# Optimization experiments

Measured on AMD Instinct MI355X. Metric: run time of the kernel, lower is better.

The kernel has to match this reference:

```python
import jax, jax.numpy as jnp
import numpy as np

WS = 8        # window_size
NH = 16       # num_heads
EPS = 1e-5    # BatchNorm eps (inference mode: running_mean=0, running_var=1)

def conv2d(x, w, padding=0, groups=1):
    return jax.lax.conv_general_dilated(
        x, w, (1, 1), [(padding, padding), (padding, padding)],
        dimension_numbers=('NCHW', 'OIHW', 'NCHW'), feature_group_count=groups)

def bn(x, gamma, beta):
    # eval-mode BatchNorm with running_mean=0, running_var=1
    return x * (gamma / jnp.sqrt(1.0 + EPS))[None, :, None, None] + beta[None, :, None, None]

def avgpool(x, kh, kw, ph, pw):
    # torch AvgPool2d with count_include_pad=True: sum over zero-padded window / (kh*kw)
    s = jax.lax.reduce_window(x, 0.0, jax.lax.add, (1, 1, kh, kw), (1, 1, 1, 1),
                              [(0, 0), (0, 0), (ph, ph), (pw, pw)])
    return s / float(kh * kw)

def rel_pos_index(ws):
    coords = np.stack(np.meshgrid(np.arange(ws), np.arange(ws), indexing='ij')).reshape(2, -1)
    rel = (coords[:, :, None] - coords[:, None, :]).transpose(1, 2, 0) + (ws - 1)
    return (rel[..., 0] * (2 * ws - 1) + rel[..., 1]).reshape(-1)

def hge_kernels(W):
    # build 4 directional Sobel kernels + Gaussian-Laplacian from learned scalars
    S0, S45, S90 = W[:, :, 0, 0], W[:, :, 0, 1], W[:, :, 0, 2]
    S135, GL = W[:, :, 1, 0], W[:, :, 2, 2]
    z = jnp.zeros_like(S0)
    k3 = lambda rows: jnp.stack([jnp.stack(r, -1) for r in rows], -2)  # [O,I,3,3]
    w0 = k3([[S0, 2*S0, S0], [z, z, z], [-S0, -2*S0, -S0]])
    w45 = k3([[2*S45, S45, z], [S45, z, -S45], [z, -S45, -2*S45]])
    w90 = k3([[S90, z, -S90], [2*S90, z, -2*S90], [S90, z, -S90]])
    w135 = k3([[z, -S135, -2*S135], [S135, z, -S135], [2*S135, S135, z]])
    a1 = GL * 4.0; a2 = -a1 / 8.0; a3 = -a1 / 16.0
    wGL = jnp.zeros(S0.shape + (5, 5), S0.dtype)
    for i, j, v in [(0,2,a3),(1,1,a3),(1,2,a2),(1,3,a3),(2,0,a3),(2,1,a2),(2,2,a1),
                    (2,3,a2),(2,4,a3),(3,1,a3),(3,2,a2),(3,3,a3),(4,2,a3)]:
        wGL = wGL.at[:, :, i, j].set(v)
    return w0, w45, w90, w135, wGL

def forward(x, ca_h1, ca_w1, ca_fh, ca_fw, l1_w, l1_g, l1_b, l2_w, l2_g, l2_b,
            hge_w, hge_fc_w, hge_fc_b, qkv_w, rel_table, proj_dw, proj_g, proj_b, proj_pw):
    B, C, H, W = x.shape
    d = C // NH
    scale = d ** -0.5
    # --- CA block: coordinate attention (1x1 convs on H- and W-pooled features) ---
    cm = lambda w, t: jnp.einsum('oc,bc...->bo...', w, t)
    s_h = jax.nn.sigmoid(cm(ca_fh, cm(ca_h1, x.mean(3))))   # [B,C,H]
    s_w = jax.nn.sigmoid(cm(ca_fw, cm(ca_w1, x.mean(2))))   # [B,C,W]
    x = x * s_h[:, :, :, None] * s_w[:, :, None, :]
    # --- local branch: 1x1 ConvBN + 3x3 ConvBN + HGE edge operator ---
    local = bn(conv2d(x, l2_w), l2_g, l2_b) + bn(conv2d(x, l1_w, padding=1), l1_g, l1_b)
    w0, w45, w90, w135, wGL = hge_kernels(hge_w)
    feats = jnp.concatenate([conv2d(x, w0, 1), conv2d(x, w45, 1), conv2d(x, w90, 1),
                             conv2d(x, w135, 1), conv2d(x, wGL, 2)], axis=1)  # [B,5C,H,W]
    local = local + conv2d(feats, hge_fc_w) + hge_fc_b[None, :, None, None]
    # --- windowed attention ---
    ph, pw = (-H) % WS, (-W) % WS
    if ph or pw:
        x = jnp.pad(x, ((0, 0), (0, 0), (0, ph), (0, pw)), mode='reflect')
    Hp, Wp = x.shape[2], x.shape[3]
    hh, ww = Hp // WS, Wp // WS
    qkv = conv2d(x, qkv_w)                                   # [B,3C,Hp,Wp]
    qkv = qkv.reshape(B, 3, NH, d, hh, WS, ww, WS)
    qkv = qkv.transpose(1, 0, 4, 6, 2, 5, 7, 3).reshape(3, B * hh * ww, NH, WS * WS, d)
    q, k, v = qkv[0], qkv[1], qkv[2]
    bias = rel_table[rel_pos_index(WS)].reshape(WS * WS, WS * WS, NH).transpose(2, 0, 1)
    dots = jnp.einsum('wnid,wnjd->wnij', q, k) * scale + bias[None]
    attn = jax.nn.softmax(dots, axis=-1)
    o = jnp.einsum('wnij,wnjd->wnid', attn, v)
    o = o.reshape(B, hh, ww, NH, WS, WS, d).transpose(0, 3, 6, 1, 4, 2, 5)
    o = o.reshape(B, C, Hp, Wp)[:, :, :H, :W]
    # --- directional average pooling of attention output ---
    ox = avgpool(jnp.pad(o, ((0, 0), (0, 0), (0, 1), (0, 0)), mode='reflect'), WS, 1, WS // 2 - 1, 0)
    oy = avgpool(jnp.pad(o, ((0, 0), (0, 0), (0, 0), (0, 1)), mode='reflect'), 1, WS, 0, WS // 2 - 1)
    out = ox + oy + local
    # --- pad_out + separable ConvBN projection (depthwise k=ws -> BN -> 1x1) ---
    out = jnp.pad(out, ((0, 0), (0, 0), (0, 1), (0, 1)), mode='reflect')
    out = conv2d(out, proj_dw, padding=(WS - 1) // 2, groups=C)
    out = bn(out, proj_g, proj_b)
    out = conv2d(out, proj_pw)
    return out[:, :, :H, :W]

def setup_inputs() -> dict:
    key = jax.random.key(0)
    ks = jax.random.split(key, 20)
    C = 128
    f32 = jnp.float32
    n = lambda k, sh, s: jax.random.normal(k, sh, f32) * s
    return {
        'x': jax.random.normal(ks[0], (2, C, 256, 256), f32),
        'ca_h1': n(ks[1], (C, C), 0.05), 'ca_w1': n(ks[2], (C, C), 0.05),
        'ca_fh': n(ks[3], (C, C), 0.05), 'ca_fw': n(ks[4], (C, C), 0.05),
        'l1_w': n(ks[5], (C, C, 3, 3), 0.03),
        'l1_g': 1.0 + n(ks[6], (C,), 0.02), 'l1_b': n(ks[7], (C,), 0.02),
        'l2_w': n(ks[8], (C, C, 1, 1), 0.09),
        'l2_g': 1.0 + n(ks[9], (C,), 0.02), 'l2_b': n(ks[10], (C,), 0.02),
        'hge_w': n(ks[11], (C, C, 3, 3), 0.02),
        'hge_fc_w': n(ks[12], (C, 5 * C, 1, 1), 0.02), 'hge_fc_b': n(ks[13], (C,), 0.02),
        'qkv_w': n(ks[14], (3 * C, C, 1, 1), 0.05),
        'rel_table': n(ks[15], ((2 * WS - 1) ** 2, NH), 0.02),
        'proj_dw': n(ks[16], (C, 1, WS, WS), 0.05),
        'proj_g': 1.0 + n(ks[17], (C,), 0.02), 'proj_b': n(ks[18], (C,), 0.02),
        'proj_pw': n(ks[19], (C, C, 1, 1), 0.05),
    }

def reference(x, ca_h1, ca_w1, ca_fh, ca_fw, l1_w, l1_g, l1_b, l2_w, l2_g, l2_b,
              hge_w, hge_fc_w, hge_fc_b, qkv_w, rel_table, proj_dw, proj_g, proj_b, proj_pw):
    return forward(x, ca_h1, ca_w1, ca_fh, ca_fw, l1_w, l1_g, l1_b, l2_w, l2_g, l2_b,
                   hge_w, hge_fc_w, hge_fc_b, qkv_w, rel_table, proj_dw, proj_g, proj_b, proj_pw)
```

## Files before the change

kernel.cpp:

```cpp
#include <hip/hip_runtime.h>

#define BB 2
#define CC 128
#define HWSZ 65536
#define RSQE 0.9999950000374997f
#define ATT_SCALE 0.35355339059327373f

typedef unsigned short u16;
using short8 = __attribute__((ext_vector_type(8))) short;
using f32x4  = __attribute__((ext_vector_type(4))) float;

#if defined(__has_builtin)
# if __has_builtin(__builtin_amdgcn_fdot2_f32_bf16)
#  define HAVE_DOT2 1
# endif
#endif

__device__ __forceinline__ float b2f(u16 u){
  return __uint_as_float(((unsigned int)u) << 16);
}
__device__ __forceinline__ u16 f2b(float f){
  unsigned int v = __float_as_uint(f);
  unsigned int r = (v + 0x7FFFu + ((v >> 16) & 1u)) >> 16;
  return (u16)r;
}

__device__ const int c_DI[13] = {-2,-1,-1,-1, 0, 0,0,0,0, 1,1,1, 2};
__device__ const int c_DJ[13] = { 0,-1, 0, 1,-2,-1,0,1,2,-1,0,1, 0};

__global__ void k_detect(const u16* __restrict__ xr, int* __restrict__ flag){
  __shared__ int ws_[4];
  int tid = threadIdx.x;
  int cnt = 0;
  for (int i = 0; i < 16; ++i){
    u16 u = xr[tid*16 + i];
    int e = (u >> 7) & 0xFF;
    cnt += (e < 100 || e > 141) ? 1 : 0;
  }
  #pragma unroll
  for (int off = 32; off > 0; off >>= 1) cnt += __shfl_down(cnt, off, 64);
  if ((tid & 63) == 0) ws_[tid >> 6] = cnt;
  __syncthreads();
  if (tid == 0) *flag = (ws_[0]+ws_[1]+ws_[2]+ws_[3] > 64) ? 1 : 0;
}

__global__ void k_ingest4(const void* __restrict__ src, u16* __restrict__ dst,
                          int n4, const int* __restrict__ flag){
  int i = blockIdx.x * 256 + threadIdx.x;
  if (i >= n4) return;
  if (*flag){
    float4 f = ((const float4*)src)[i];
    ushort4 r; r.x=f2b(f.x); r.y=f2b(f.y); r.z=f2b(f.z); r.w=f2b(f.w);
    ((ushort4*)dst)[i] = r;
  } else {
    ((ushort4*)dst)[i] = ((const ushort4*)src)[i];
  }
}

struct PtrL { const void* p[19]; };

__global__ void k_ingest_w(PtrL pl, u16* __restrict__ dst, const int* __restrict__ flag){
  const int ends[19] = {16384,32768,49152,65536,212992,213120,213248,229632,229760,
                        229888,377344,459264,459392,508544,512144,520336,520464,520592,536976};
  int g = blockIdx.x * 256 + threadIdx.x;
  int idx = g * 4;
  if (idx >= 536976) return;
  int seg = 0, start = 0;
  #pragma unroll
  for (int s = 0; s < 19; ++s){ if (idx >= ends[s]){ seg = s+1; start = ends[s]; } }
  int local = idx - start;
  const void* sp = pl.p[seg];
  if (*flag){
    float4 f = ((const float4*)sp)[local >> 2];
    ushort4 r; r.x=f2b(f.x); r.y=f2b(f.y); r.z=f2b(f.z); r.w=f2b(f.w);
    *(ushort4*)(dst + idx) = r;
  } else {
    *(ushort4*)(dst + idx) = ((const ushort4*)sp)[local >> 2];
  }
}

__global__ void k_prep_A(const u16* __restrict__ fh, const u16* __restrict__ h1,
                         const u16* __restrict__ fw, const u16* __restrict__ w1,
                         const u16* __restrict__ l1b, const u16* __restrict__ l2b,
                         const u16* __restrict__ fcb,
                         float* __restrict__ A_h, float* __restrict__ A_w,
                         float* __restrict__ biasK){
  int idx = blockIdx.x * 256 + threadIdx.x;
  int o = idx >> 7, c = idx & 127;
  float ah = 0.f, aw = 0.f;
  for (int m = 0; m < 128; ++m){
    ah += b2f(fh[o*128 + m]) * b2f(h1[m*128 + c]);
    aw += b2f(fw[o*128 + m]) * b2f(w1[m*128 + c]);
  }
  A_h[idx] = ah; A_w[idx] = aw;
  if (c == 0) biasK[o] = b2f(l1b[o]) + b2f(l2b[o]) + b2f(fcb[o]);
}

__global__ void k_prep_rel(const u16* __restrict__ rel, float* __restrict__ relo){
  int idx = blockIdx.x * 256 + threadIdx.x;
  if (idx >= 3600) return;
  int head = idx / 225, i = idx - head*225;
  relo[idx] = b2f(rel[i*16 + head]);
}

__global__ void k_prep_K(const u16* __restrict__ hge_w, const u16* __restrict__ fc_w,
                         const u16* __restrict__ l1_w, const u16* __restrict__ l1_g,
                         const u16* __restrict__ l2_w, const u16* __restrict__ l2_g,
                         u16* __restrict__ Kwb){
  int idx = blockIdx.x * 256 + threadIdx.x;
  int o = idx >> 7, c = idx & 127;
  float m0=0.f, m45=0.f, m90=0.f, m135=0.f, mgl=0.f;
  const u16* fo = fc_w + o*640;
  for (int m = 0; m < 128; ++m){
    const u16* hw9 = hge_w + (size_t)(m*128 + c)*9;
    m0   += b2f(fo[m      ]) * b2f(hw9[0]);
    m45  += b2f(fo[128 + m]) * b2f(hw9[1]);
    m90  += b2f(fo[256 + m]) * b2f(hw9[2]);
    m135 += b2f(fo[384 + m]) * b2f(hw9[3]);
    mgl  += b2f(fo[512 + m]) * b2f(hw9[8]);
  }
  float g1 = b2f(l1_g[o]) * RSQE;
  float g2 = b2f(l2_g[o]) * RSQE;
  float l1v[9];
  #pragma unroll
  for (int t = 0; t < 9; ++t) l1v[t] = b2f(l1_w[(size_t)idx*9 + t]) * g1;
  float l2v = b2f(l2_w[idx]) * g2;
  float kp[13];
  kp[0]  = -0.25f*mgl;
  kp[1]  =  m0 + 2.f*m45 + m90              - 0.25f*mgl + l1v[0];
  kp[2]  =  2.f*m0 + m45 - m135             - 0.50f*mgl + l1v[1];
  kp[3]  =  m0 - m90 - 2.f*m135             - 0.25f*mgl + l1v[2];
  kp[4]  = -0.25f*mgl;
  kp[5]  =  m45 + 2.f*m90 + m135            - 0.50f*mgl + l1v[3];
  kp[6]  =  4.f*mgl + l1v[4] + l2v;
  kp[7]  = -m45 - 2.f*m90 - m135            - 0.50f*mgl + l1v[5];
  kp[8]  = -0.25f*mgl;
  kp[9]  = -m0 + m90 + 2.f*m135             - 0.25f*mgl + l1v[6];
  kp[10] = -2.f*m0 - m45 + m135             - 0.50f*mgl + l1v[7];
  kp[11] = -m0 - 2.f*m45 - m90              - 0.25f*mgl + l1v[8];
  kp[12] = -0.25f*mgl;
  #pragma unroll
  for (int t = 0; t < 13; ++t) Kwb[t*16384 + idx] = f2b(kp[t]);
}

__global__ void k_means(const u16* __restrict__ x, float* __restrict__ mh, float* __restrict__ mw){
  __shared__ float colpart[4][256];
  int c = blockIdx.x, b = blockIdx.y;
  const u16* xp = x + (size_t)(b*CC + c)*HWSZ;
  int tid = threadIdx.x, lane = tid & 63, wv = tid >> 6;
  float c0=0.f,c1=0.f,c2=0.f,c3=0.f;
  for (int r = 0; r < 64; ++r){
    int h = wv*64 + r;
    ushort4 u = *(const ushort4*)(xp + h*256 + lane*4);
    float v0=b2f(u.x), v1=b2f(u.y), v2=b2f(u.z), v3=b2f(u.w);
    c0+=v0; c1+=v1; c2+=v2; c3+=v3;
    float rs = v0+v1+v2+v3;
    #pragma unroll
    for (int off = 32; off > 0; off >>= 1) rs += __shfl_down(rs, off, 64);
    if (lane == 0) mh[(size_t)(b*CC + c)*256 + h] = rs * (1.0f/256.0f);
  }
  colpart[wv][lane*4+0]=c0; colpart[wv][lane*4+1]=c1;
  colpart[wv][lane*4+2]=c2; colpart[wv][lane*4+3]=c3;
  __syncthreads();
  mw[(size_t)(b*CC + c)*256 + tid] =
    (colpart[0][tid]+colpart[1][tid]+colpart[2][tid]+colpart[3][tid]) * (1.0f/256.0f);
}

__global__ void k_sig(const float* __restrict__ A_h, const float* __restrict__ A_w,
                      const float* __restrict__ mh, const float* __restrict__ mw,
                      float* __restrict__ s_h, float* __restrict__ s_w){
  int o = blockIdx.x, b = blockIdx.y, sel = blockIdx.z, t = threadIdx.x;
  const float* A = sel ? A_w : A_h;
  const float* m = sel ? mw : mh;
  float* s = sel ? s_w : s_h;
  float acc = 0.f;
  for (int c = 0; c < 128; ++c)
    acc += A[o*128 + c] * m[(size_t)(b*CC + c)*256 + t];
  s[(size_t)(b*CC + o)*256 + t] = 1.0f / (1.0f + __expf(-acc));
}

__global__ void k_scale2cl(const u16* __restrict__ cx, const float* __restrict__ s_h,
                           const float* __restrict__ s_w, u16* __restrict__ xcl){
  __shared__ u16 t[16][136];
  int b = blockIdx.z >> 8, h = blockIdx.z & 255;
  int w0 = blockIdx.x * 16;
  int tid = threadIdx.x;
  int ic = tid >> 1, wseg = (tid & 1) * 8;
  uint4 v = *(const uint4*)(cx + (size_t)(b*CC + ic)*HWSZ + h*256 + w0 + wseg);
  float sh = s_h[(size_t)(b*CC + ic)*256 + h];
  const float* swp = s_w + (size_t)(b*CC + ic)*256 + w0 + wseg;
  float4 swa = *(const float4*)swp;
  float4 swb = *(const float4*)(swp + 4);
  u16 tmp[8]; *(uint4*)tmp = v;
  t[wseg+0][ic] = f2b(b2f(tmp[0])*sh*swa.x);
  t[wseg+1][ic] = f2b(b2f(tmp[1])*sh*swa.y);
  t[wseg+2][ic] = f2b(b2f(tmp[2])*sh*swa.z);
  t[wseg+3][ic] = f2b(b2f(tmp[3])*sh*swa.w);
  t[wseg+4][ic] = f2b(b2f(tmp[4])*sh*swb.x);
  t[wseg+5][ic] = f2b(b2f(tmp[5])*sh*swb.y);
  t[wseg+6][ic] = f2b(b2f(tmp[6])*sh*swb.z);
  t[wseg+7][ic] = f2b(b2f(tmp[7])*sh*swb.w);
  __syncthreads();
  int w = tid >> 4, part = (tid & 15) * 8;
  uint4 o = *(const uint4*)&t[w][part];
  *(uint4*)(xcl + ((size_t)(b*256 + h)*256 + (w0 + w))*128 + part) = o;
}

__global__ void k_cf2cl(const u16* __restrict__ src, u16* __restrict__ dst){
  __shared__ u16 t[16][136];
  int b = blockIdx.z >> 8, h = blockIdx.z & 255;
  int w0 = blockIdx.x * 16;
  int tid = threadIdx.x;
  int ic = tid >> 1, wseg = (tid & 1) * 8;
  uint4 v = *(const uint4*)(src + (size_t)(b*CC + ic)*HWSZ + h*256 + w0 + wseg);
  u16 tmp[8]; *(uint4*)tmp = v;
  #pragma unroll
  for (int k = 0; k < 8; ++k) t[wseg + k][ic] = tmp[k];
  __syncthreads();
  int w = tid >> 4, part = (tid & 15) * 8;
  uint4 o = *(const uint4*)&t[w][part];
  *(uint4*)(dst + ((size_t)(b*256 + h)*256 + (w0 + w))*128 + part) = o;
}

__launch_bounds__(256)
__global__ void k_conv5t(const u16* __restrict__ xcl, const u16* __restrict__ Kwb,
                         const float* __restrict__ biasK, u16* __restrict__ outp){
  __shared__ u16 As[128][136];
  __shared__ u16 Bs[128][136];
  int tid = threadIdx.x;
  int wv = tid >> 6, lane = tid & 63;
  int q = lane >> 4, l16 = lane & 15;
  int pt0 = blockIdx.x;
  int pt = (pt0 & 7) * 128 + (pt0 >> 3);
  int b = pt >> 9, h = (pt >> 1) & 255, w0 = (pt & 1) << 7;
  int mrow = (wv & 1) << 6, nrow = (wv >> 1) << 6;
  const u16* xb_b = xcl + (size_t)b*HWSZ*128;
  f32x4 acc[4][4];
  #pragma unroll
  for (int mt = 0; mt < 4; ++mt)
    #pragma unroll
    for (int nt = 0; nt < 4; ++nt) acc[mt][nt] = (f32x4){0.f,0.f,0.f,0.f};

  for (int t = 0; t < 13; ++t){
    int di = c_DI[t], dj = c_DJ[t];
    int hh2 = h + di;
    bool rowok = (unsigned)hh2 < 256u;
    const u16* rowbase = xb_b + (size_t)(rowok ? hh2 : 0)*256*128;
    const u16* Bb = Kwb + t*16384;
    __syncthreads();
    #pragma unroll
    for (int i = 0; i < 8; ++i){
      int seg = i*256 + tid;
      int px = seg >> 4, chunk = (seg & 15) << 3;
      int col = w0 + dj + px;
      uint4 v = {0,0,0,0};
      if (rowok && (unsigned)col < 256u)
        v = *(const uint4*)(rowbase + col*128 + chunk);
      *(uint4*)&As[px][chunk] = v;
      *(uint4*)&Bs[px][chunk] = *(const uint4*)(Bb + seg*8);
    }
    __syncthreads();
    #pragma unroll
    for (int kc = 0; kc < 4; ++kc){
      short8 af[4], bf[4];
      #pragma unroll
      for (int mt = 0; mt < 4; ++mt) af[mt] = *(const short8*)&As[mrow + mt*16 + l16][kc*32 + q*8];
      #pragma unroll
      for (int nt = 0; nt < 4; ++nt) bf[nt] = *(const short8*)&Bs[nrow + nt*16 + l16][kc*32 + q*8];
      #pragma unroll
      for (int mt = 0; mt < 4; ++mt)
        #pragma unroll
        for (int nt = 0; nt < 4; ++nt)
          acc[mt][nt] = __builtin_amdgcn_mfma_f32_16x16x32_bf16(af[mt], bf[nt], acc[mt][nt], 0, 0, 0);
    }
  }
  #pragma unroll
  for (int nt = 0; nt < 4; ++nt){
    int n = nrow + nt*16 + l16;
    float bv = biasK[n];
    size_t cbase = (size_t)(b*CC + n)*HWSZ + h*256 + w0;
    #pragma unroll
    for (int mt = 0; mt < 4; ++mt){
      int m = mrow + mt*16 + q*4;
      ushort4 st;
      st.x = f2b(acc[mt][nt][0] + bv);
      st.y = f2b(acc[mt][nt][1] + bv);
      st.z = f2b(acc[mt][nt][2] + bv);
      st.w = f2b(acc[mt][nt][3] + bv);
      *(ushort4*)(outp + cbase + m) = st;
    }
  }
}

__launch_bounds__(256)
__global__ void k_mgemm(const u16* __restrict__ Xcl, const u16* __restrict__ W,
                        u16* __restrict__ Y, float* __restrict__ Yf,
                        const int* __restrict__ flag, int nsel, int mode){
  __shared__ u16 As[128][136];
  __shared__ u16 Bs[128][136];
  int tid = threadIdx.x;
  int wv = tid >> 6, lane = tid & 63;
  int q = lane >> 4, l16 = lane & 15;
  int pt = blockIdx.x;
  int b = pt >> 9, h = (pt >> 1) & 255, w0 = (pt & 1) << 7;
  int mrow = (wv & 1) << 6, nrow = (wv >> 1) << 6;
  const u16* Abase = Xcl + ((size_t)(b*256 + h)*256 + w0)*128;
  #pragma unroll
  for (int i = 0; i < 8; ++i){
    int seg = i*256 + tid;
    *(uint4*)&As[seg >> 4][(seg & 15) << 3] = *(const uint4*)(Abase + seg*8);
  }
  for (int sel = 0; sel < nsel; ++sel){
    __syncthreads();
    const u16* Wb = W + sel*16384;
    #pragma unroll
    for (int i = 0; i < 8; ++i){
      int seg = i*256 + tid;
      *(uint4*)&Bs[seg >> 4][(seg & 15) << 3] = *(const uint4*)(Wb + seg*8);
    }
    __syncthreads();
    f32x4 acc[4][4];
    #pragma unroll
    for (int mt = 0; mt < 4; ++mt)
      #pragma unroll
      for (int nt = 0; nt < 4; ++nt) acc[mt][nt] = (f32x4){0.f,0.f,0.f,0.f};
    #pragma unroll
    for (int kc = 0; kc < 4; ++kc){
      short8 af[4], bf[4];
      #pragma unroll
      for (int mt = 0; mt < 4; ++mt) af[mt] = *(const short8*)&As[mrow + mt*16 + l16][kc*32 + q*8];
      #pragma unroll
      for (int nt = 0; nt < 4; ++nt) bf[nt] = *(const short8*)&Bs[nrow + nt*16 + l16][kc*32 + q*8];
      #pragma unroll
      for (int mt = 0; mt < 4; ++mt)
        #pragma unroll
        for (int nt = 0; nt < 4; ++nt)
          acc[mt][nt] = __builtin_amdgcn_mfma_f32_16x16x32_bf16(af[mt], bf[nt], acc[mt][nt], 0, 0, 0);
    }
    if (mode == 0){
      __syncthreads();
      #pragma unroll
      for (int mt = 0; mt < 4; ++mt){
        int m0i = mrow + mt*16 + q*4;
        #pragma unroll
        for (int nt = 0; nt < 4; ++nt){
          int n = nrow + nt*16 + l16;
          Bs[m0i+0][n] = f2b(acc[mt][nt][0]);
          Bs[m0i+1][n] = f2b(acc[mt][nt][1]);
          Bs[m0i+2][n] = f2b(acc[mt][nt][2]);
          Bs[m0i+3][n] = f2b(acc[mt][nt][3]);
        }
      }
      __syncthreads();
      int win = tid >> 4, head = tid & 15;
      size_t obase = (((((size_t)b*32 + (h >> 3))*32 + (w0 >> 3) + win)*3 + sel)*16 + head)*512
                     + (size_t)(h & 7)*64;
      #pragma unroll
      for (int pj = 0; pj < 8; ++pj){
        uint4 vv = *(const uint4*)&Bs[win*8 + pj][head*8];
        *(uint4*)(Y + obase + pj*8) = vv;
      }
    } else {
      int f32o = (Yf != nullptr) && (*flag != 0);
      #pragma unroll
      for (int nt = 0; nt < 4; ++nt){
        int n = nrow + nt*16 + l16;
        size_t cbase = (size_t)(b*CC + n)*HWSZ + h*256 + w0;
        #pragma unroll
        for (int mt = 0; mt < 4; ++mt){
          int m = mrow + mt*16 + q*4;
          if (f32o){
            float4 st; st.x=acc[mt][nt][0]; st.y=acc[mt][nt][1];
            st.z=acc[mt][nt][2]; st.w=acc[mt][nt][3];
            *(float4*)(Yf + cbase + m) = st;
          } else {
            ushort4 st;
            st.x = f2b(acc[mt][nt][0]); st.y = f2b(acc[mt][nt][1]);
            st.z = f2b(acc[mt][nt][2]); st.w = f2b(acc[mt][nt][3]);
            *(ushort4*)(Y + cbase + m) = st;
          }
        }
      }
    }
  }
}

__launch_bounds__(256)
__global__ void k_attn3(const u16* __restrict__ qkvw, const float* __restrict__ relo,
                        u16* __restrict__ obuf){
  __shared__ float relf[228];
  __shared__ u16  kls[4][64][8];
  __shared__ float vls[4][64][8];
  int tid = threadIdx.x, wv = tid >> 6, lane = tid & 63;
  int b = blockIdx.z >> 4, head = blockIdx.z & 15;
  int hh = blockIdx.y, ww = blockIdx.x * 4 + wv;

  for (int e = tid; e < 225; e += 256) relf[e] = relo[head*225 + e];

  size_t base = (((size_t)b*32 + hh)*32 + ww)*3*8192 + (size_t)head*512;
  uint4 qv = *(const uint4*)(qkvw + base + lane*8);
  *(uint4*)&kls[wv][lane][0] = *(const uint4*)(qkvw + base + 8192 + lane*8);
  {
    uint4 raw = *(const uint4*)(qkvw + base + 16384 + lane*8);
    u16 tv[8]; *(uint4*)tv = raw;
    float4 lo, hi;
    lo.x=b2f(tv[0]); lo.y=b2f(tv[1]); lo.z=b2f(tv[2]); lo.w=b2f(tv[3]);
    hi.x=b2f(tv[4]); hi.y=b2f(tv[5]); hi.z=b2f(tv[6]); hi.w=b2f(tv[7]);
    *(float4*)&vls[wv][lane][0] = lo;
    *(float4*)&vls[wv][lane][4] = hi;
  }
  __syncthreads();

  int qi = lane >> 3, qj = lane & 7;
  const float* rbase = relf + (qi + 7)*15 + (qj + 7);
  float s[64];
#if HAVE_DOT2
  typedef __bf16 bf2 __attribute__((ext_vector_type(2)));
  bf2 q0 = __builtin_bit_cast(bf2, qv.x), q1 = __builtin_bit_cast(bf2, qv.y);
  bf2 q2 = __builtin_bit_cast(bf2, qv.z), q3 = __builtin_bit_cast(bf2, qv.w);
  #pragma unroll
  for (int kp = 0; kp < 64; ++kp){
    uint4 kv = *(const uint4*)&kls[wv][kp][0];
    float d = __builtin_amdgcn_fdot2_f32_bf16(q3, __builtin_bit_cast(bf2, kv.w), 0.f, false);
    d = __builtin_amdgcn_fdot2_f32_bf16(q2, __builtin_bit_cast(bf2, kv.z), d, false);
    d = __builtin_amdgcn_fdot2_f32_bf16(q1, __builtin_bit_cast(bf2, kv.y), d, false);
    d = __builtin_amdgcn_fdot2_f32_bf16(q0, __builtin_bit_cast(bf2, kv.x), d, false);
    s[kp] = fmaf(d, ATT_SCALE, rbase[-((kp>>3)*15 + (kp&7))]);
  }
#else
  float qf[8];
  { u16 tq[8]; *(uint4*)tq = qv;
    #pragma unroll
    for (int d = 0; d < 8; ++d) qf[d] = b2f(tq[d]); }
  #pragma unroll
  for (int kp = 0; kp < 64; ++kp){
    uint4 kv = *(const uint4*)&kls[wv][kp][0];
    u16 tk[8]; *(uint4*)tk = kv;
    float d = 0.f;
    #pragma unroll
    for (int dd = 0; dd < 8; ++dd) d = fmaf(qf[dd], b2f(tk[dd]), d);
    s[kp] = fmaf(d, ATT_SCALE, rbase[-((kp>>3)*15 + (kp&7))]);
  }
#endif
  float t16[16];
  #pragma unroll
  for (int i = 0; i < 16; ++i)
    t16[i] = fmaxf(fmaxf(s[i], s[i+16]), fmaxf(s[i+32], s[i+48]));
  float mx = t16[0];
  #pragma unroll
  for (int i = 1; i < 16; ++i) mx = fmaxf(mx, t16[i]);
  #pragma unroll
  for (int kp = 0; kp < 64; ++kp) s[kp] = __expf(s[kp] - mx);
  #pragma unroll
  for (int i = 0; i < 16; ++i)
    t16[i] = (s[i] + s[i+16]) + (s[i+32] + s[i+48]);
  float sum = t16[0];
  #pragma unroll
  for (int i = 1; i < 16; ++i) sum += t16[i];
  float inv = 1.0f / sum;
  float ov[8] = {0.f,0.f,0.f,0.f,0.f,0.f,0.f,0.f};
  #pragma unroll
  for (int kp = 0; kp < 64; ++kp){
    float4 va = *(const float4*)&vls[wv][kp][0];
    float4 vb = *(const float4*)&vls[wv][kp][4];
    float pp = s[kp];
    ov[0] = fmaf(pp, va.x, ov[0]); ov[1] = fmaf(pp, va.y, ov[1]);
    ov[2] = fmaf(pp, va.z, ov[2]); ov[3] = fmaf(pp, va.w, ov[3]);
    ov[4] = fmaf(pp, vb.x, ov[4]); ov[5] = fmaf(pp, vb.y, ov[5]);
    ov[6] = fmaf(pp, vb.z, ov[6]); ov[7] = fmaf(pp, vb.w, ov[7]);
  }
  size_t obase = (size_t)(b*CC + head*8)*HWSZ + (size_t)(hh*8 + qi)*256 + ww*8 + qj;
  #pragma unroll
  for (int d = 0; d < 8; ++d)
    obuf[obase + (size_t)d*HWSZ] = f2b(ov[d] * inv);
}

__launch_bounds__(256)
__global__ void k_pool2(const u16* __restrict__ obuf, u16* __restrict__ localb){
  __shared__ u16 t[71][88];
  int bc = blockIdx.z;
  int h0 = blockIdx.y * 64, w0 = blockIdx.x * 64;
  int tid = threadIdx.x;
  const u16* op = obuf + (size_t)bc * HWSZ;

  for (int e = tid; e < 710; e += 256){
    int tr = e / 10, ci = e - tr*10;
    int gt = h0 - 3 + tr;
    if (gt == 256) gt = 254;
    bool rv = (unsigned)gt <= 255u;
    int g0 = w0 - 8 + ci*8;
    uint4 v = {0,0,0,0};
    if (rv){
      if (g0 >= 0 && g0 <= 248){
        v = *(const uint4*)(op + gt*256 + g0);
      } else {
        u16 tmp[8];
        #pragma unroll
        for (int j = 0; j < 8; ++j){
          int g = g0 + j;
          if (g == 256) g = 254;
          tmp[j] = ((unsigned)g <= 255u) ? op[gt*256 + g] : (u16)0;
        }
        v = *(const uint4*)tmp;
      }
    }
    *(uint4*)&t[tr][ci*8] = v;
  }
  __syncthreads();

  int ty = tid >> 4, tx = tid & 15;
  int r0 = ty*4, c0 = tx*4;
  float sxv[4][4];
  #pragma unroll
  for (int c = 0; c < 4; ++c){
    float col[11];
    #pragma unroll
    for (int i = 0; i < 11; ++i) col[i] = b2f(t[r0+i][c0+8+c]);
    float s = ((col[0]+col[1])+(col[2]+col[3]))+((col[4]+col[5])+(col[6]+col[7]));
    sxv[0][c] = s;
    s += col[8]  - col[0]; sxv[1][c] = s;
    s += col[9]  - col[1]; sxv[2][c] = s;
    s += col[10] - col[2]; sxv[3][c] = s;
  }
  #pragma unroll
  for (int r = 0; r < 4; ++r){
    int rr = r0 + r;
    float pre[11];
    #pragma unroll
    for (int j = 0; j < 11; ++j) pre[j] = b2f(t[rr+3][c0+5+j]);
    float sy0 = ((pre[0]+pre[1])+(pre[2]+pre[3]))+((pre[4]+pre[5])+(pre[6]+pre[7]));
    float sy1 = sy0 + pre[8]  - pre[0];
    float sy2 = sy1 + pre[9]  - pre[1];
    float sy3 = sy2 + pre[10] - pre[2];
    size_t base = (size_t)bc*HWSZ + (size_t)(h0+rr)*256 + (w0+c0);
    ushort4 lv = *(const ushort4*)(localb + base);
    ushort4 st;
    st.x = f2b((sxv[r][0]+sy0)*0.125f + b2f(lv.x));
    st.y = f2b((sxv[r][1]+sy1)*0.125f + b2f(lv.y));
    st.z = f2b((sxv[r][2]+sy2)*0.125f + b2f(lv.z));
    st.w = f2b((sxv[r][3]+sy3)*0.125f + b2f(lv.w));
    *(ushort4*)(localb + base) = st;
  }
}

__launch_bounds__(256)
__global__ void k_dw2(const u16* __restrict__ u_, const u16* __restrict__ dww,
                      const u16* __restrict__ g, const u16* __restrict__ bta,
                      u16* __restrict__ dwout){
  __shared__ u16 xt[71][152];
  int c = blockIdx.z & 127, b = blockIdx.z >> 7;
  int h0 = blockIdx.y * 64, w0 = blockIdx.x * 128;
  int tid = threadIdx.x;
  const u16* up = u_ + (size_t)(b*CC + c)*HWSZ;

  for (int e = tid; e < 71*18; e += 256){
    int tr = e / 18, ci = e - tr*18;
    int gt = h0 - 3 + tr;
    if (gt == 256) gt = 254;
    int g0 = w0 - 8 + ci*8;
    uint4 v = {0,0,0,0};
    if ((unsigned)gt <= 255u){
      if (g0 >= 0 && g0 <= 248){
        v = *(const uint4*)(up + gt*256 + g0);
      } else {
        u16 tmp[8];
        #pragma unroll
        for (int j = 0; j < 8; ++j){
          int gw = g0 + j;
          if (gw == 256) gw = 254;
          tmp[j] = ((unsigned)gw <= 255u) ? up[gt*256 + gw] : (u16)0;
        }
        v = *(const uint4*)tmp;
      }
    }
    *(uint4*)&xt[tr][ci*8] = v;
  }

#if HAVE_DOT2
  typedef __bf16 bf2v __attribute__((ext_vector_type(2)));
  unsigned int wp[32];
  {
    const uint4* wsrc = (const uint4*)(dww + c*64);
    #pragma unroll
    for (int t = 0; t < 8; ++t){
      uint4 v = wsrc[t];
      wp[t*4+0]=v.x; wp[t*4+1]=v.y; wp[t*4+2]=v.z; wp[t*4+3]=v.w;
    }
  }
#else
  float wf[64];
  {
    const u16* wsrc = dww + c*64;
    #pragma unroll
    for (int t = 0; t < 64; ++t) wf[t] = b2f(wsrc[t]);
  }
#endif
  __syncthreads();

  int tx = tid & 15, ty = tid >> 4;
  int r0 = ty*4;
  int cb = tx*8;
  float acc[4][8];
  #pragma unroll
  for (int r = 0; r < 4; ++r)
    #pragma unroll
    for (int k = 0; k < 8; ++k) acc[r][k] = 0.f;

  #pragma unroll
  for (int i = 0; i < 11; ++i){
    const u16* rowp = &xt[r0 + i][cb + 4];
    uint2 av = *(const uint2*)(rowp);
    uint4 mv = *(const uint4*)(rowp + 4);
    uint2 zv = *(const uint2*)(rowp + 12);
    unsigned int d0=av.x, d1=av.y, d2=mv.x, d3=mv.y, d4=mv.z, d5=mv.w, d6=zv.x, d7=zv.y;
    unsigned int dd[8] = {d0,d1,d2,d3,d4,d5,d6,d7};
#if HAVE_DOT2
    unsigned int xp[15];
    #pragma unroll
    for (int t = 1; t < 15; ++t)
      xp[t] = (t & 1) ? ((dd[t>>1] >> 16) | (dd[(t>>1)+1] << 16)) : dd[t>>1];
    #pragma unroll
    for (int dr = 0; dr < 4; ++dr){
      int wr = i - dr;
      if (wr >= 0 && wr < 8){
        #pragma unroll
        for (int k = 0; k < 8; ++k){
          float s = acc[dr][k];
          #pragma unroll
          for (int p = 0; p < 4; ++p)
            s = __builtin_amdgcn_fdot2_f32_bf16(
                  __builtin_bit_cast(bf2v, wp[wr*4+p]),
                  __builtin_bit_cast(bf2v, xp[1+k+2*p]), s, false);
          acc[dr][k] = s;
        }
      }
    }
#else
    float xw[16];
    #pragma unroll
    for (int t = 1; t < 16; ++t){
      unsigned int w32 = dd[t>>1];
      xw[t] = __uint_as_float((t & 1) ? (w32 & 0xFFFF0000u) : (w32 << 16));
    }
    #pragma unroll
    for (int dr = 0; dr < 4; ++dr){
      int wr = i - dr;
      if (wr >= 0 && wr < 8){
        #pragma unroll
        for (int k = 0; k < 8; ++k){
          float s = acc[dr][k];
          #pragma unroll
          for (int j = 0; j < 8; ++j)
            s = fmaf(wf[wr*8+j], xw[1+k+j], s);
          acc[dr][k] = s;
        }
      }
    }
#endif
  }

  float scale = b2f(g[c]) * RSQE;
  float bb = b2f(bta[c]);
  size_t obase = (size_t)(b*CC + c)*HWSZ + (size_t)(h0 + r0)*256 + w0 + cb;
  #pragma unroll
  for (int r = 0; r < 4; ++r){
    u16 po[8];
    #pragma unroll
    for (int k = 0; k < 8; ++k) po[k] = f2b(acc[r][k]*scale + bb);
    *(uint4*)(dwout + obase + (size_t)r*256) = *(uint4*)po;
  }
}

extern "C" void kernel_launch(void* const* d_in, const int* in_sizes, int n_in,
                              void* d_out, int out_size, void* d_ws, size_t ws_size,
                              hipStream_t stream) {
  char* p = (char*)d_ws;
  u16* cx     = (u16*)p; p += 33554432;
  u16* xcl    = (u16*)p; p += 33554432;
  u16* qkvb   = (u16*)p; p += 100663296;
  u16* cw     = (u16*)p; p += 1074176;
  float* A_h    = (float*)p; p += 65536;
  float* A_w    = (float*)p; p += 65536;
  u16*  Kwb     = (u16*)p;  p += 425984;
  float* biasK  = (float*)p; p += 1024;
  float* mh     = (float*)p; p += 262144;
  float* mw     = (float*)p; p += 262144;
  float* s_h    = (float*)p; p += 262144;
  float* s_w    = (float*)p; p += 262144;
  int* flag     = (int*)p;   p += 256;
  float* relo   = (float*)p; p += 16384;

  u16* localb = (u16*)d_out;
  u16* qkvw   = qkvb;
  u16* obuf   = cx;
  u16* dwbuf  = qkvb;
  u16* dwcl   = xcl;

  const int O_h1=0, O_w1=16384, O_fh=32768, O_fw=49152, O_l1w=65536, O_l1g=212992,
            O_l1b=213120, O_l2w=213248, O_l2g=229632, O_l2b=229760, O_hge=229888,
            O_fcw=377344, O_fcb=459264, O_qkvw=459392, O_rel=508544, O_dw=512144,
            O_pg=520336, O_pb=520464, O_pw=520592;

  k_detect<<<1, 256, 0, stream>>>((const u16*)d_in[0], flag);
  k_ingest4<<<16384, 256, 0, stream>>>(d_in[0], cx, 4194304, flag);
  PtrL pl;
  for (int i = 0; i < 19; ++i) pl.p[i] = d_in[i+1];
  k_ingest_w<<<525, 256, 0, stream>>>(pl, cw, flag);

  k_prep_A<<<64, 256, 0, stream>>>(cw+O_fh, cw+O_h1, cw+O_fw, cw+O_w1,
                                   cw+O_l1b, cw+O_l2b, cw+O_fcb, A_h, A_w, biasK);
  k_prep_rel<<<15, 256, 0, stream>>>(cw+O_rel, relo);
  k_prep_K<<<64, 256, 0, stream>>>(cw+O_hge, cw+O_fcw, cw+O_l1w, cw+O_l1g,
                                   cw+O_l2w, cw+O_l2g, Kwb);
  k_means<<<dim3(128, 2), 256, 0, stream>>>(cx, mh, mw);
  k_sig<<<dim3(128, 2, 2), 256, 0, stream>>>(A_h, A_w, mh, mw, s_h, s_w);
  k_scale2cl<<<dim3(16, 1, 512), 256, 0, stream>>>(cx, s_h, s_w, xcl);

  k_conv5t<<<1024, 256, 0, stream>>>(xcl, Kwb, biasK, localb);
  k_mgemm<<<1024, 256, 0, stream>>>(xcl, cw+O_qkvw, qkvw, nullptr, flag, 3, 0);
  k_attn3<<<dim3(8, 32, 32), 256, 0, stream>>>(qkvw, relo, obuf);
  k_pool2<<<dim3(4, 4, 256), 256, 0, stream>>>(obuf, localb);
  k_dw2<<<dim3(2, 4, 256), 256, 0, stream>>>(localb, cw+O_dw, cw+O_pg, cw+O_pb, dwbuf);
  k_cf2cl<<<dim3(16, 1, 512), 256, 0, stream>>>(dwbuf, dwcl);
  k_mgemm<<<1024, 256, 0, stream>>>(dwcl, cw+O_pw, (u16*)d_out, (float*)d_out, flag, 1, 1);
}
```

Before: 571.8 us.

## Load conv tiles directly into LDS with XOR-swizzled layout and skip out-of-range rows

The 13-tap conv GEMM kernel now fills its A and B tiles with global_load_lds direct-to-LDS copies instead of staging through registers. Padded LDS rows are replaced by an XOR swizzle on the 16-byte chunks to avoid bank conflicts, and out-of-bounds columns read from a small zeroed page. Taps whose source row falls outside the image are skipped entirely. This is meant to cut register pressure and VGPR round-trips in the load phase, at the cost of an extra tiny kernel launch that zeroes the page.

```diff
diff --git a/kernel.cpp b/kernel.cpp
--- a/kernel.cpp
+++ b/kernel.cpp
@@ -23,6 +23,12 @@
   unsigned int v = __float_as_uint(f);
   unsigned int r = (v + 0x7FFFu + ((v >> 16) & 1u)) >> 16;
   return (u16)r;
+}
+
+__device__ __forceinline__ void gload16(const u16* g, u16* l){
+  __builtin_amdgcn_global_load_lds(
+      (__attribute__((address_space(1))) void*)(g),
+      (__attribute__((address_space(3))) void*)(l), 16, 0, 0);
 }
 
 __device__ const int c_DI[13] = {-2,-1,-1,-1, 0, 0,0,0,0, 1,1,1, 2};
@@ -43,6 +49,8 @@
   __syncthreads();
   if (tid == 0) *flag = (ws_[0]+ws_[1]+ws_[2]+ws_[3] > 64) ? 1 : 0;
 }
+
+__global__ void k_zero(uint4* zp){ zp[threadIdx.x] = (uint4){0,0,0,0}; }
 
 __global__ void k_ingest4(const void* __restrict__ src, u16* __restrict__ dst,
                           int n4, const int* __restrict__ flag){
@@ -223,10 +231,11 @@
 }
 
 __launch_bounds__(256)
-__global__ void k_conv5t(const u16* __restrict__ xcl, const u16* __restrict__ Kwb,
-                         const float* __restrict__ biasK, u16* __restrict__ outp){
-  __shared__ u16 As[128][136];
-  __shared__ u16 Bs[128][136];
+__global__ void k_conv5g(const u16* __restrict__ xcl, const u16* __restrict__ Kwb,
+                         const float* __restrict__ biasK, const u16* __restrict__ zp,
+                         u16* __restrict__ outp){
+  __shared__ u16 As[128*128];
+  __shared__ u16 Bs[128*128];
   int tid = threadIdx.x;
   int wv = tid >> 6, lane = tid & 63;
   int q = lane >> 4, l16 = lane & 15;
@@ -241,32 +250,40 @@
     #pragma unroll
     for (int nt = 0; nt < 4; ++nt) acc[mt][nt] = (f32x4){0.f,0.f,0.f,0.f};
 
+  int px_t   = tid >> 4;
+  int c16p_t = tid & 15;
+  int swzread = (l16 & 7) << 3;
+
   for (int t = 0; t < 13; ++t){
     int di = c_DI[t], dj = c_DJ[t];
     int hh2 = h + di;
-    bool rowok = (unsigned)hh2 < 256u;
-    const u16* rowbase = xb_b + (size_t)(rowok ? hh2 : 0)*256*128;
+    if ((unsigned)hh2 >= 256u) continue;
+    const u16* rowbase = xb_b + (size_t)hh2*32768;
     const u16* Bb = Kwb + t*16384;
     __syncthreads();
     #pragma unroll
     for (int i = 0; i < 8; ++i){
-      int seg = i*256 + tid;
-      int px = seg >> 4, chunk = (seg & 15) << 3;
-      int col = w0 + dj + px;
-      uint4 v = {0,0,0,0};
-      if (rowok && (unsigned)col < 256u)
-        v = *(const uint4*)(rowbase + col*128 + chunk);
-      *(uint4*)&As[px][chunk] = v;
-      *(uint4*)&Bs[px][chunk] = *(const uint4*)(Bb + seg*8);
+      int px   = px_t + i*16;
+      int c16s = c16p_t ^ (px & 7);
+      int col  = w0 + dj + px;
+      const u16* asrc = ((unsigned)col < 256u) ? (rowbase + col*128 + c16s*8) : zp;
+      const u16* bsrc = Bb + px*128 + c16s*8;
+      u16* albase = &As[(i*256 + wv*64) * 8];
+      u16* blbase = &Bs[(i*256 + wv*64) * 8];
+      gload16(asrc, albase);
+      gload16(bsrc, blbase);
     }
     __syncthreads();
     #pragma unroll
     for (int kc = 0; kc < 4; ++kc){
+      int swz = ((kc*4 + q) << 3) ^ swzread;
       short8 af[4], bf[4];
       #pragma unroll
-      for (int mt = 0; mt < 4; ++mt) af[mt] = *(const short8*)&As[mrow + mt*16 + l16][kc*32 + q*8];
-      #pragma unroll
-      for (int nt = 0; nt < 4; ++nt) bf[nt] = *(const short8*)&Bs[nrow + nt*16 + l16][kc*32 + q*8];
+      for (int mt = 0; mt < 4; ++mt)
+        af[mt] = *(const short8*)&As[(mrow + mt*16 + l16)*128 + swz];
+      #pragma unroll
+      for (int nt = 0; nt < 4; ++nt)
+        bf[nt] = *(const short8*)&Bs[(nrow + nt*16 + l16)*128 + swz];
       #pragma unroll
       for (int mt = 0; mt < 4; ++mt)
         #pragma unroll
@@ -689,6 +706,7 @@
   float* s_w    = (float*)p; p += 262144;
   int* flag     = (int*)p;   p += 256;
   float* relo   = (float*)p; p += 16384;
+  u16* zpage    = (u16*)p;   p += 4096;
 
   u16* localb = (u16*)d_out;
   u16* qkvw   = qkvb;
@@ -702,6 +720,7 @@
             O_pg=520336, O_pb=520464, O_pw=520592;
 
   k_detect<<<1, 256, 0, stream>>>((const u16*)d_in[0], flag);
+  k_zero<<<1, 256, 0, stream>>>((uint4*)zpage);
   k_ingest4<<<16384, 256, 0, stream>>>(d_in[0], cx, 4194304, flag);
   PtrL pl;
   for (int i = 0; i < 19; ++i) pl.p[i] = d_in[i+1];
@@ -716,7 +735,7 @@
   k_sig<<<dim3(128, 2, 2), 256, 0, stream>>>(A_h, A_w, mh, mw, s_h, s_w);
   k_scale2cl<<<dim3(16, 1, 512), 256, 0, stream>>>(cx, s_h, s_w, xcl);
 
-  k_conv5t<<<1024, 256, 0, stream>>>(xcl, Kwb, biasK, localb);
+  k_conv5g<<<1024, 256, 0, stream>>>(xcl, Kwb, biasK, zpage, localb);
   k_mgemm<<<1024, 256, 0, stream>>>(xcl, cw+O_qkvw, qkvw, nullptr, flag, 3, 0);
   k_attn3<<<dim3(8, 32, 32), 256, 0, stream>>>(qkvw, relo, obuf);
   k_pool2<<<dim3(4, 4, 256), 256, 0, stream>>>(obuf, localb);
```

Result: faster. 540.2 us (-5.5%).
